# Performance work log

Hardware: AMD Instinct MI355X
Metric: run time of the kernel (lower is better)

Reference implementation:

```python
import jax, jax.numpy as jnp
import numpy as np

N = 500_000   # nodes
E = 16_000_000  # edges
G = 5_000     # graphs
H = 64        # hidden_channels
BN_EPS = 1e-5


def setup_inputs() -> dict:
    key = jax.random.key(0)
    ks = jax.random.split(key, 8)
    f32 = jnp.float32
    return {
        "x": jax.random.normal(ks[0], (N, 4), f32),
        "eps": jnp.zeros((), f32),
        "w1": jax.random.normal(ks[1], (4, 2 * H), f32) * 0.5,
        "b1": jnp.zeros((2 * H,), f32),
        "g1": jnp.ones((2 * H,), f32),
        "be1": jnp.zeros((2 * H,), f32),
        "m1": jnp.zeros((2 * H,), f32),
        "v1": jnp.ones((2 * H,), f32),
        "w2": jax.random.normal(ks[2], (2 * H, H), f32) * 0.1,
        "b2": jnp.zeros((H,), f32),
        "g2": jnp.ones((H,), f32),
        "be2": jnp.zeros((H,), f32),
        "m2": jnp.zeros((H,), f32),
        "v2": jnp.ones((H,), f32),
        "w3": jax.random.normal(ks[3], (H, 2), f32) * 0.1,
        "b3": jnp.zeros((2,), f32),
        "edge_index": jax.random.randint(ks[4], (2, E), 0, N, dtype=jnp.int64) if jax.config.jax_enable_x64 else jax.random.randint(ks[4], (2, E), 0, N, dtype=jnp.int32),
        "batch": jnp.sort(jax.random.randint(ks[5], (N,), 0, G, dtype=jnp.int32)),
    }


def _bn_eval(h, g, be, m, v):
    # BatchNorm1d in eval mode: affine transform with running stats
    return (h - m) * (g * jax.lax.rsqrt(v + BN_EPS)) + be


def reference(x, eps, w1, b1, g1, be1, m1, v1, w2, b2, g2, be2, m2, v2,
              w3, b3, edge_index, batch):
    src, dst = edge_index[0], edge_index[1]
    # GINConv: h_i = nn((1+eps)*x_i + sum_{j->i} x_j)   (adj_t @ x)
    agg = jax.ops.segment_sum(x[src], dst, num_segments=N)  # [N,4]
    h = (1.0 + eps) * x + agg
    # MLP: Linear-BN-ReLU-Linear-BN-ReLU
    h = jax.nn.relu(_bn_eval(h @ w1 + b1, g1, be1, m1, v1))   # [N,128]
    h = jax.nn.relu(_bn_eval(h @ w2 + b2, g2, be2, m2, v2))   # [N,64]
    # dropout is identity at inference
    # global_mean_pool over graphs
    sums = jax.ops.segment_sum(h, batch, num_segments=G)      # [G,64]
    cnt = jax.ops.segment_sum(jnp.ones((N, 1), h.dtype), batch, num_segments=G)
    pooled = sums / jnp.maximum(cnt, 1.0)
    logits = pooled @ w3 + b3                                 # [G,2]
    return jax.nn.log_softmax(logits, axis=-1)
```

## Files before the change

### kernel.cpp

```cpp
#include <hip/hip_runtime.h>
#include <hip/hip_fp16.h>

#define N_NODES  500000
#define N_EDGES  16000000
#define N_GRAPHS 5000

#define NBIN  512
#define BSZN  1024
#define CH    16384
#define NCH   977

#define FXS   262144.0f
#define FXI   3.814697265625e-06f

#define WS_AGG     0
#define WS_SUMS    2000000
#define WS_CNT     2320000
#define WS_W1F     2325008
#define WS_B1F     2325520
#define WS_W2F     2325648
#define WS_B2F     2333840
#define WS_HIST    2333904
#define WS_XH      WS_HIST
#define WS_BTOT    3334352
#define WS_BSTART  3334864
#define WS_CSR     3335377
#define WS_TOTAL_ELEMS 19335377

typedef __attribute__((ext_vector_type(8))) short short8;
typedef __attribute__((ext_vector_type(4))) float f32x4;

static __device__ __forceinline__ unsigned short bf16r(float f) {
    unsigned int u = __float_as_uint(f);
    u = u + 0x7FFFu + ((u >> 16) & 1u);
    return (unsigned short)(u >> 16);
}

__global__ void k_prep(const float* __restrict__ w1, const float* __restrict__ b1,
                       const float* __restrict__ g1, const float* __restrict__ be1,
                       const float* __restrict__ m1, const float* __restrict__ v1,
                       const float* __restrict__ w2, const float* __restrict__ b2,
                       const float* __restrict__ g2, const float* __restrict__ be2,
                       const float* __restrict__ m2, const float* __restrict__ v2,
                       float* __restrict__ ws) {
    int t = threadIdx.x;
    if (t < 128) {
        float s = g1[t] * rsqrtf(v1[t] + 1e-5f);
        ws[WS_B1F + t] = (b1[t] - m1[t]) * s + be1[t];
        for (int c = 0; c < 4; ++c)
            ws[WS_W1F + t * 4 + c] = w1[c * 128 + t] * s;
    }
    if (t < 64) {
        float s = g2[t] * rsqrtf(v2[t] + 1e-5f);
        ws[WS_B2F + t] = (b2[t] - m2[t]) * s + be2[t];
        unsigned short* w2t = (unsigned short*)(ws + WS_W2F);
        for (int j = 0; j < 128; ++j)
            w2t[t * 128 + j] = bf16r(w2[j * 64 + t] * s);
    }
}

__global__ __launch_bounds__(256) void k_xhalf(const float4* __restrict__ x4,
                                               uint2* __restrict__ xh) {
    int i = blockIdx.x * 256 + threadIdx.x;
    if (i >= N_NODES) return;
    float4 v = x4[i];
    __half2 a = __floats2half2_rn(v.x, v.y);
    __half2 b = __floats2half2_rn(v.z, v.w);
    uint2 p;
    p.x = *(unsigned int*)&a;
    p.y = *(unsigned int*)&b;
    xh[i] = p;
}

__global__ __launch_bounds__(256) void k_e1_hist(const int* __restrict__ ei,
                                                 int* __restrict__ hist) {
    __shared__ int h[NBIN];
    int t = threadIdx.x, blk = blockIdx.x;
    for (int i = t; i < NBIN; i += 256) h[i] = 0;
    __syncthreads();
    int base = blk * CH;
    int nE = min(CH, N_EDGES - base);
    const int4* d4 = (const int4*)(ei + N_EDGES + base);
    for (int i = t; i < (nE >> 2); i += 256) {
        int4 d = d4[i];
        atomicAdd(&h[d.x >> 10], 1);
        atomicAdd(&h[d.y >> 10], 1);
        atomicAdd(&h[d.z >> 10], 1);
        atomicAdd(&h[d.w >> 10], 1);
    }
    __syncthreads();
    for (int i = t; i < NBIN; i += 256) hist[blk * NBIN + i] = h[i];
}

__global__ __launch_bounds__(256) void k_e2a_scan(int* __restrict__ hist,
                                                  int* __restrict__ binTotal) {
    __shared__ int buf[NCH];
    int t = threadIdx.x, bin = blockIdx.x;
    for (int i = t; i < NCH; i += 256) buf[i] = hist[i * NBIN + bin];
    __syncthreads();
    if (t == 0) {
        int run = 0;
        for (int i = 0; i < NCH; ++i) { int v = buf[i]; buf[i] = run; run += v; }
        binTotal[bin] = run;
    }
    __syncthreads();
    for (int i = t; i < NCH; i += 256) hist[i * NBIN + bin] = buf[i];
}

__global__ __launch_bounds__(256) void k_e2b_scan(const int* __restrict__ binTotal,
                                                  int* __restrict__ binStart) {
    __shared__ int buf[NBIN];
    int t = threadIdx.x;
    for (int i = t; i < NBIN; i += 256) buf[i] = binTotal[i];
    __syncthreads();
    if (t == 0) {
        int run = 0;
        for (int i = 0; i < NBIN; ++i) { int v = buf[i]; buf[i] = run; run += v; }
        binStart[NBIN] = run;
    }
    __syncthreads();
    for (int i = t; i < NBIN; i += 256) binStart[i] = buf[i];
}

#define E3T 512
__global__ __launch_bounds__(E3T) void k_e3_sort(const int* __restrict__ ei,
                                                 const int* __restrict__ hist,
                                                 const int* __restrict__ binStart,
                                                 unsigned int* __restrict__ csr) {
    __shared__ unsigned int ebuf[CH];
    __shared__ int lhist[NBIN];
    __shared__ int lbase[NBIN];
    __shared__ int gbase[NBIN];
    __shared__ int cursor[NBIN];
    __shared__ int wtot[8], woff[8];
    int t = threadIdx.x, c = blockIdx.x;

    lhist[t] = 0;
    __syncthreads();

    int base = c * CH;
    int nE = min(CH, N_EDGES - base);
    for (int i = t; i < nE; i += E3T) {
        int d = ei[N_EDGES + base + i];
        atomicAdd(&lhist[d >> 10], 1);
    }
    __syncthreads();
    int v = lhist[t];
    int inc = v;
    #pragma unroll
    for (int dlt = 1; dlt < 64; dlt <<= 1) {
        int n = __shfl_up(inc, dlt, 64);
        if ((t & 63) >= dlt) inc += n;
    }
    if ((t & 63) == 63) wtot[t >> 6] = inc;
    __syncthreads();
    if (t == 0) { int r = 0; for (int w = 0; w < 8; ++w) { woff[w] = r; r += wtot[w]; } }
    __syncthreads();
    int excl = inc - v + woff[t >> 6];
    lbase[t]  = excl;
    cursor[t] = excl;
    gbase[t]  = binStart[t] + hist[c * NBIN + t];
    __syncthreads();
    for (int i = t; i < nE; i += E3T) {
        int e = base + i;
        int s = ei[e];
        int d = ei[N_EDGES + e];
        int bin = d >> 10;
        int pos = atomicAdd(&cursor[bin], 1);
        ebuf[pos] = ((unsigned int)s << 10) | (unsigned int)(d & 1023u);
    }
    __syncthreads();
    int grp = t >> 5, lane = t & 31;
    for (int b = grp; b < NBIN; b += 16) {
        int n  = lhist[b];
        int lb = lbase[b];
        int gb = gbase[b];
        for (int j = lane; j < n; j += 32)
            csr[gb + j] = ebuf[lb + j];
    }
}

__global__ __launch_bounds__(1024) void k_e4_agg(const unsigned int* __restrict__ csr,
                                                 const int* __restrict__ binStart,
                                                 const uint2* __restrict__ xh,
                                                 float* __restrict__ agg) {
    __shared__ int aggs_i[BSZN * 4];
    int t = threadIdx.x, bin = blockIdx.x;
    for (int i = t; i < BSZN * 4; i += 1024) aggs_i[i] = 0;
    __syncthreads();
    int start = binStart[bin];
    int end   = binStart[bin + 1];
    #pragma unroll 4
    for (int e = start + t; e < end; e += 1024) {
        unsigned int v = __builtin_nontemporal_load(&csr[e]);
        int src = (int)(v >> 10);
        int loc = (int)(v & 1023u);
        uint2 p = xh[src];
        __half2 ab = *(__half2*)&p.x;
        __half2 cd = *(__half2*)&p.y;
        float2 f0 = __half22float2(ab);
        float2 f1 = __half22float2(cd);
        atomicAdd(&aggs_i[0 * BSZN + loc], __float2int_rn(f0.x * FXS));
        atomicAdd(&aggs_i[1 * BSZN + loc], __float2int_rn(f0.y * FXS));
        atomicAdd(&aggs_i[2 * BSZN + loc], __float2int_rn(f1.x * FXS));
        atomicAdd(&aggs_i[3 * BSZN + loc], __float2int_rn(f1.y * FXS));
    }
    __syncthreads();
    int nodeBase = bin * BSZN;
    if (nodeBase >= N_NODES) return;
    int nv = min(BSZN, N_NODES - nodeBase) * 4;
    for (int i = t; i < nv; i += 1024) {
        int loc = i >> 2, c = i & 3;
        agg[nodeBase * 4 + i] = (float)aggs_i[c * BSZN + loc] * FXI;
    }
}

__global__ __launch_bounds__(256) void k_edge(const int* __restrict__ ei,
                                              const float4* __restrict__ x4,
                                              float* __restrict__ agg) {
    int e = blockIdx.x * 256 + threadIdx.x;
    if (e >= N_EDGES) return;
    int s = ei[e];
    int d = ei[N_EDGES + e];
    float4 v = x4[s];
    atomicAdd(&agg[d * 4 + 0], v.x);
    atomicAdd(&agg[d * 4 + 1], v.y);
    atomicAdd(&agg[d * 4 + 2], v.z);
    atomicAdd(&agg[d * 4 + 3], v.w);
}

__global__ __launch_bounds__(512) void k_node(const float4* __restrict__ x4,
                                              const float4* __restrict__ agg4,
                                              const int* __restrict__ batch,
                                              const float* __restrict__ epsp,
                                              const float* __restrict__ ws,
                                              float* __restrict__ sums,
                                              float* __restrict__ cnt) {
    __shared__ float w1s4[4 * 516];
    __shared__ float b1s[128];
    __shared__ float b2s[64];
    __shared__ float h2t[8][16][68];
    __shared__ int   bshW[128];

    int tid  = threadIdx.x;
    int wave = tid >> 6;
    int l    = tid & 63;
    int cl   = l & 15;
    int q8   = l >> 4;

    for (int i = tid; i < 2048; i += 512)
        w1s4[(i >> 9) * 516 + (i & 511)] = ws[WS_W1F + (i & 511)];
    if (tid < 128) b1s[tid] = ws[WS_B1F + tid];
    if (tid < 64)  b2s[tid] = ws[WS_B2F + tid];

    const unsigned short* w2t = (const unsigned short*)(ws + WS_W2F);
    short8 bfr[4][4];
    #pragma unroll
    for (int nt = 0; nt < 4; ++nt)
        #pragma unroll
        for (int ks = 0; ks < 4; ++ks)
            bfr[nt][ks] = *(const short8*)(w2t + (nt * 16 + cl) * 128 + ks * 32 + q8 * 8);

    __syncthreads();

    int tilebase = blockIdx.x * 128 + wave * 16;
    int node = tilebase + cl;
    bool valid = node < N_NODES;
    float4 xi = valid ? x4[node]   : make_float4(0.f, 0.f, 0.f, 0.f);
    float4 ai = valid ? agg4[node] : make_float4(0.f, 0.f, 0.f, 0.f);
    int bn = valid ? batch[node] : -1;
    if (l < 16) bshW[wave * 16 + l] = bn;
    float ep = 1.0f + epsp[0];
    float hx = ep * xi.x + ai.x;
    float hy = ep * xi.y + ai.y;
    float hz = ep * xi.z + ai.z;
    float hw = ep * xi.w + ai.w;

    f32x4 acc[4];
    #pragma unroll
    for (int nt = 0; nt < 4; ++nt) acc[nt] = (f32x4){0.f, 0.f, 0.f, 0.f};

    #pragma unroll
    for (int ks = 0; ks < 4; ++ks) {
        short8 afrag;
        #pragma unroll
        for (int e = 0; e < 8; ++e) {
            int j = ks * 32 + q8 * 8 + e;
            const float4 wr = *(const float4*)&w1s4[q8 * 516 + j * 4];
            float h1 = fmaf(hx, wr.x, fmaf(hy, wr.y, fmaf(hz, wr.z, fmaf(hw, wr.w, b1s[j]))));
            h1 = fmaxf(h1, 0.0f);
            afrag[e] = (short)bf16r(h1);
        }
        #pragma unroll
        for (int nt = 0; nt < 4; ++nt)
            acc[nt] = __builtin_amdgcn_mfma_f32_16x16x32_bf16(afrag, bfr[nt][ks], acc[nt], 0, 0, 0);
    }

    float h2v[4][4];
    #pragma unroll
    for (int nt = 0; nt < 4; ++nt) {
        float b2v = b2s[nt * 16 + cl];
        #pragma unroll
        for (int r = 0; r < 4; ++r)
            h2v[nt][r] = fmaxf(acc[nt][r] + b2v, 0.0f);
    }

    int firstb = __shfl(bn, 0);
    bool uni = __all(bn == firstb) && (firstb >= 0);
    if (uni) {
        float s[4];
        #pragma unroll
        for (int nt = 0; nt < 4; ++nt) {
            float v = h2v[nt][0] + h2v[nt][1] + h2v[nt][2] + h2v[nt][3];
            v += __shfl_xor(v, 16);
            v += __shfl_xor(v, 32);
            s[nt] = v;
        }
        if (l < 16) {
            #pragma unroll
            for (int nt = 0; nt < 4; ++nt)
                atomicAdd(&sums[firstb * 64 + nt * 16 + l], s[nt]);
        }
        if (l == 0) atomicAdd(&cnt[firstb], 16.0f);
    } else {
        #pragma unroll
        for (int nt = 0; nt < 4; ++nt)
            #pragma unroll
            for (int r = 0; r < 4; ++r)
                h2t[wave][q8 * 4 + r][nt * 16 + cl] = h2v[nt][r];
        int kout = l;
        float a = 0.f, c = 0.f;
        int cur = -1;
        for (int n = 0; n < 16; ++n) {
            int bn2 = bshW[wave * 16 + n];
            if (bn2 != cur) {
                if (cur >= 0) {
                    atomicAdd(&sums[cur * 64 + kout], a);
                    if (l == 0) atomicAdd(&cnt[cur], c);
                }
                a = 0.f; c = 0.f; cur = bn2;
            }
            if (bn2 >= 0) { a += h2t[wave][n][kout]; c += 1.f; }
        }
        if (cur >= 0) {
            atomicAdd(&sums[cur * 64 + kout], a);
            if (l == 0) atomicAdd(&cnt[cur], c);
        }
    }
}

__global__ __launch_bounds__(256) void k_head(const float* __restrict__ sums,
                                              const float* __restrict__ cnt,
                                              const float* __restrict__ w3,
                                              const float* __restrict__ b3,
                                              float* __restrict__ out) {
    int g = blockIdx.x * 256 + threadIdx.x;
    if (g >= N_GRAPHS) return;
    float ic = 1.0f / fmaxf(cnt[g], 1.0f);
    float l0 = b3[0], l1 = b3[1];
    #pragma unroll 8
    for (int k = 0; k < 64; ++k) {
        float p = sums[g * 64 + k] * ic;
        l0 = fmaf(p, w3[k * 2 + 0], l0);
        l1 = fmaf(p, w3[k * 2 + 1], l1);
    }
    float m = fmaxf(l0, l1);
    float lse = m + logf(expf(l0 - m) + expf(l1 - m));
    out[g * 2 + 0] = l0 - lse;
    out[g * 2 + 1] = l1 - lse;
}

extern "C" void kernel_launch(void* const* d_in, const int* in_sizes, int n_in,
                              void* d_out, int out_size, void* d_ws, size_t ws_size,
                              hipStream_t stream) {
    const float* x   = (const float*)d_in[0];
    const float* eps = (const float*)d_in[1];
    const float* w1  = (const float*)d_in[2];
    const float* b1  = (const float*)d_in[3];
    const float* g1  = (const float*)d_in[4];
    const float* be1 = (const float*)d_in[5];
    const float* m1  = (const float*)d_in[6];
    const float* v1  = (const float*)d_in[7];
    const float* w2  = (const float*)d_in[8];
    const float* b2  = (const float*)d_in[9];
    const float* g2  = (const float*)d_in[10];
    const float* be2 = (const float*)d_in[11];
    const float* m2  = (const float*)d_in[12];
    const float* v2  = (const float*)d_in[13];
    const float* w3  = (const float*)d_in[14];
    const float* b3  = (const float*)d_in[15];
    const int*   ei  = (const int*)d_in[16];
    const int*   batch = (const int*)d_in[17];

    float* ws = (float*)d_ws;
    int*   wsi = (int*)d_ws;

    k_prep<<<1, 128, 0, stream>>>(w1, b1, g1, be1, m1, v1, w2, b2, g2, be2, m2, v2, ws);

    if (ws_size >= (size_t)WS_TOTAL_ELEMS * 4) {
        hipMemsetAsync(ws + WS_SUMS, 0, (size_t)(320000 + 5000) * sizeof(float), stream);

        k_e1_hist<<<NCH, 256, 0, stream>>>(ei, wsi + WS_HIST);
        k_e2a_scan<<<NBIN, 256, 0, stream>>>(wsi + WS_HIST, wsi + WS_BTOT);
        k_e2b_scan<<<1, 256, 0, stream>>>(wsi + WS_BTOT, wsi + WS_BSTART);
        k_e3_sort<<<NCH, E3T, 0, stream>>>(ei, wsi + WS_HIST, wsi + WS_BSTART,
                                           (unsigned int*)(wsi + WS_CSR));
        k_xhalf<<<(N_NODES + 255) / 256, 256, 0, stream>>>((const float4*)x,
                                                           (uint2*)(wsi + WS_XH));
        k_e4_agg<<<NBIN, 1024, 0, stream>>>((const unsigned int*)(wsi + WS_CSR),
                                            wsi + WS_BSTART,
                                            (const uint2*)(wsi + WS_XH), ws + WS_AGG);
    } else {
        hipMemsetAsync(ws, 0, (size_t)(2000000 + 320000 + 5000) * sizeof(float), stream);
        k_edge<<<(N_EDGES + 255) / 256, 256, 0, stream>>>(ei, (const float4*)x, ws + WS_AGG);
    }

    k_node<<<(N_NODES + 127) / 128, 512, 0, stream>>>(
        (const float4*)x, (const float4*)(ws + WS_AGG), batch, eps, ws,
        ws + WS_SUMS, ws + WS_CNT);

    k_head<<<(N_GRAPHS + 255) / 256, 256, 0, stream>>>(
        ws + WS_SUMS, ws + WS_CNT, w3, b3, (float*)d_out);
}
```

Baseline: 309.0 us.

## Replace per-chunk histogram scan with atomic bin totals and global cursors

The per-chunk bin histogram matrix and its column-wise serial scan kernel are removed. The histogram kernel now atomically accumulates global bin totals, a single parallel-scan kernel computes bin starts and cursors, and each sort block claims its slice of every bin with an atomicAdd on the global cursor. This drops one kernel launch and the strided scan over 977x512 counts, but makes edge order within a bin nondeterministic, which is harmless because aggregation uses integer atomics. The aggregation loop unroll also rises from 4 to 8.

Result: slower. 318.6 us (+3.1%).

```diff
diff --git a/kernel.cpp b/kernel.cpp
--- a/kernel.cpp
+++ b/kernel.cpp
@@ -20,12 +20,12 @@
 #define WS_B1F     2325520
 #define WS_W2F     2325648
 #define WS_B2F     2333840
-#define WS_HIST    2333904
-#define WS_XH      WS_HIST
-#define WS_BTOT    3334352
-#define WS_BSTART  3334864
-#define WS_CSR     3335377
-#define WS_TOTAL_ELEMS 19335377
+#define WS_XH      2333904
+#define WS_BTOT    3333904
+#define WS_BSTART  3334416
+#define WS_GCUR    3334929
+#define WS_CSR     3335441
+#define WS_TOTAL_ELEMS 19335441
 
 typedef __attribute__((ext_vector_type(8))) short short8;
 typedef __attribute__((ext_vector_type(4))) float f32x4;
@@ -44,6 +44,8 @@
                        const float* __restrict__ m2, const float* __restrict__ v2,
                        float* __restrict__ ws) {
     int t = threadIdx.x;
+    int* wsi = (int*)ws;
+    for (int i = t; i < NBIN; i += 128) wsi[WS_BTOT + i] = 0;
     if (t < 128) {
         float s = g1[t] * rsqrtf(v1[t] + 1e-5f);
         ws[WS_B1F + t] = (b1[t] - m1[t]) * s + be1[t];
@@ -72,8 +74,8 @@
     xh[i] = p;
 }
 
-__global__ __launch_bounds__(256) void k_e1_hist(const int* __restrict__ ei,
-                                                 int* __restrict__ hist) {
+__global__ __launch_bounds__(256) void k_hist(const int* __restrict__ ei,
+                                              int* __restrict__ binTotal) {
     __shared__ int h[NBIN];
     int t = threadIdx.x, blk = blockIdx.x;
     for (int i = t; i < NBIN; i += 256) h[i] = 0;
@@ -89,43 +91,35 @@
         atomicAdd(&h[d.w >> 10], 1);
     }
     __syncthreads();
-    for (int i = t; i < NBIN; i += 256) hist[blk * NBIN + i] = h[i];
-}
-
-__global__ __launch_bounds__(256) void k_e2a_scan(int* __restrict__ hist,
-                                                  int* __restrict__ binTotal) {
-    __shared__ int buf[NCH];
-    int t = threadIdx.x, bin = blockIdx.x;
-    for (int i = t; i < NCH; i += 256) buf[i] = hist[i * NBIN + bin];
-    __syncthreads();
-    if (t == 0) {
-        int run = 0;
-        for (int i = 0; i < NCH; ++i) { int v = buf[i]; buf[i] = run; run += v; }
-        binTotal[bin] = run;
-    }
-    __syncthreads();
-    for (int i = t; i < NCH; i += 256) hist[i * NBIN + bin] = buf[i];
-}
-
-__global__ __launch_bounds__(256) void k_e2b_scan(const int* __restrict__ binTotal,
-                                                  int* __restrict__ binStart) {
-    __shared__ int buf[NBIN];
+    for (int i = t; i < NBIN; i += 256)
+        if (h[i]) atomicAdd(&binTotal[i], h[i]);
+}
+
+__global__ __launch_bounds__(512) void k_scan(const int* __restrict__ binTotal,
+                                              int* __restrict__ binStart,
+                                              int* __restrict__ gcur) {
+    __shared__ int wtot[8], woff[8];
     int t = threadIdx.x;
-    for (int i = t; i < NBIN; i += 256) buf[i] = binTotal[i];
-    __syncthreads();
-    if (t == 0) {
-        int run = 0;
-        for (int i = 0; i < NBIN; ++i) { int v = buf[i]; buf[i] = run; run += v; }
-        binStart[NBIN] = run;
-    }
-    __syncthreads();
-    for (int i = t; i < NBIN; i += 256) binStart[i] = buf[i];
+    int v = binTotal[t];
+    int inc = v;
+    #pragma unroll
+    for (int dlt = 1; dlt < 64; dlt <<= 1) {
+        int n = __shfl_up(inc, dlt, 64);
+        if ((t & 63) >= dlt) inc += n;
+    }
+    if ((t & 63) == 63) wtot[t >> 6] = inc;
+    __syncthreads();
+    if (t == 0) { int r = 0; for (int w = 0; w < 8; ++w) { woff[w] = r; r += wtot[w]; } }
+    __syncthreads();
+    int excl = inc - v + woff[t >> 6];
+    binStart[t] = excl;
+    gcur[t] = excl;
+    if (t == NBIN - 1) binStart[NBIN] = excl + v;
 }
 
 #define E3T 512
 __global__ __launch_bounds__(E3T) void k_e3_sort(const int* __restrict__ ei,
-                                                 const int* __restrict__ hist,
-                                                 const int* __restrict__ binStart,
+                                                 int* __restrict__ gcur,
                                                  unsigned int* __restrict__ csr) {
     __shared__ unsigned int ebuf[CH];
     __shared__ int lhist[NBIN];
@@ -159,7 +153,7 @@
     int excl = inc - v + woff[t >> 6];
     lbase[t]  = excl;
     cursor[t] = excl;
-    gbase[t]  = binStart[t] + hist[c * NBIN + t];
+    gbase[t] = v ? atomicAdd(&gcur[t], v) : 0;
     __syncthreads();
     for (int i = t; i < nE; i += E3T) {
         int e = base + i;
@@ -190,7 +184,7 @@
     __syncthreads();
     int start = binStart[bin];
     int end   = binStart[bin + 1];
-    #pragma unroll 4
+    #pragma unroll 8
     for (int e = start + t; e < end; e += 1024) {
         unsigned int v = __builtin_nontemporal_load(&csr[e]);
         int src = (int)(v >> 10);
@@ -400,13 +394,12 @@
     if (ws_size >= (size_t)WS_TOTAL_ELEMS * 4) {
         hipMemsetAsync(ws + WS_SUMS, 0, (size_t)(320000 + 5000) * sizeof(float), stream);
 
-        k_e1_hist<<<NCH, 256, 0, stream>>>(ei, wsi + WS_HIST);
-        k_e2a_scan<<<NBIN, 256, 0, stream>>>(wsi + WS_HIST, wsi + WS_BTOT);
-        k_e2b_scan<<<1, 256, 0, stream>>>(wsi + WS_BTOT, wsi + WS_BSTART);
-        k_e3_sort<<<NCH, E3T, 0, stream>>>(ei, wsi + WS_HIST, wsi + WS_BSTART,
-                                           (unsigned int*)(wsi + WS_CSR));
         k_xhalf<<<(N_NODES + 255) / 256, 256, 0, stream>>>((const float4*)x,
                                                            (uint2*)(wsi + WS_XH));
+        k_hist<<<NCH, 256, 0, stream>>>(ei, wsi + WS_BTOT);
+        k_scan<<<1, 512, 0, stream>>>(wsi + WS_BTOT, wsi + WS_BSTART, wsi + WS_GCUR);
+        k_e3_sort<<<NCH, E3T, 0, stream>>>(ei, wsi + WS_GCUR,
+                                           (unsigned int*)(wsi + WS_CSR));
         k_e4_agg<<<NBIN, 1024, 0, stream>>>((const unsigned int*)(wsi + WS_CSR),
                                             wsi + WS_BSTART,
                                             (const uint2*)(wsi + WS_XH), ws + WS_AGG);
```

## Halve sort chunks, parallelize scans, vectorize sort loads, split aggregation blocks

Applied to the files above, without the earlier changes.

Edge chunk size is halved so the histogram and sort stages launch twice as many blocks. The two serial single-thread prefix scans become wave-shuffle scans. The sort kernel now reads src/dst as int4, and the aggregation kernel splits each destination bin across two blocks that merge fixed-point partial sums with global integer atomics. The cost is a larger memset to zero the integer aggregation buffer, plus extra global atomics.

Result: faster. 289.4 us (-6.4%).

```diff
diff --git a/kernel.cpp b/kernel.cpp
--- a/kernel.cpp
+++ b/kernel.cpp
@@ -7,8 +7,8 @@
 
 #define NBIN  512
 #define BSZN  1024
-#define CH    16384
-#define NCH   977
+#define CH    8192
+#define NCH   1954
 
 #define FXS   262144.0f
 #define FXI   3.814697265625e-06f
@@ -94,32 +94,51 @@
 
 __global__ __launch_bounds__(256) void k_e2a_scan(int* __restrict__ hist,
                                                   int* __restrict__ binTotal) {
-    __shared__ int buf[NCH];
+    __shared__ int buf[2048];
+    __shared__ int wsum[4], woff2[4];
     int t = threadIdx.x, bin = blockIdx.x;
-    for (int i = t; i < NCH; i += 256) buf[i] = hist[i * NBIN + bin];
-    __syncthreads();
-    if (t == 0) {
-        int run = 0;
-        for (int i = 0; i < NCH; ++i) { int v = buf[i]; buf[i] = run; run += v; }
-        binTotal[bin] = run;
-    }
-    __syncthreads();
+    for (int i = t; i < 2048; i += 256)
+        buf[i] = (i < NCH) ? hist[i * NBIN + bin] : 0;
+    __syncthreads();
+    int s = 0;
+    #pragma unroll
+    for (int k = 0; k < 8; ++k) s += buf[t * 8 + k];
+    int inc = s;
+    #pragma unroll
+    for (int dlt = 1; dlt < 64; dlt <<= 1) {
+        int n = __shfl_up(inc, dlt, 64);
+        if ((t & 63) >= dlt) inc += n;
+    }
+    if ((t & 63) == 63) wsum[t >> 6] = inc;
+    __syncthreads();
+    if (t == 0) { int r = 0; for (int w = 0; w < 4; ++w) { woff2[w] = r; r += wsum[w]; } }
+    __syncthreads();
+    int run = inc - s + woff2[t >> 6];
+    #pragma unroll
+    for (int k = 0; k < 8; ++k) { int v = buf[t * 8 + k]; buf[t * 8 + k] = run; run += v; }
+    __syncthreads();
+    if (t == 0) binTotal[bin] = woff2[3] + wsum[3];
     for (int i = t; i < NCH; i += 256) hist[i * NBIN + bin] = buf[i];
 }
 
-__global__ __launch_bounds__(256) void k_e2b_scan(const int* __restrict__ binTotal,
+__global__ __launch_bounds__(512) void k_e2b_scan(const int* __restrict__ binTotal,
                                                   int* __restrict__ binStart) {
-    __shared__ int buf[NBIN];
+    __shared__ int wtot[8], woff[8];
     int t = threadIdx.x;
-    for (int i = t; i < NBIN; i += 256) buf[i] = binTotal[i];
-    __syncthreads();
-    if (t == 0) {
-        int run = 0;
-        for (int i = 0; i < NBIN; ++i) { int v = buf[i]; buf[i] = run; run += v; }
-        binStart[NBIN] = run;
-    }
-    __syncthreads();
-    for (int i = t; i < NBIN; i += 256) binStart[i] = buf[i];
+    int v = binTotal[t];
+    int inc = v;
+    #pragma unroll
+    for (int dlt = 1; dlt < 64; dlt <<= 1) {
+        int n = __shfl_up(inc, dlt, 64);
+        if ((t & 63) >= dlt) inc += n;
+    }
+    if ((t & 63) == 63) wtot[t >> 6] = inc;
+    __syncthreads();
+    if (t == 0) { int r = 0; for (int w = 0; w < 8; ++w) { woff[w] = r; r += wtot[w]; } }
+    __syncthreads();
+    int excl = inc - v + woff[t >> 6];
+    binStart[t] = excl;
+    if (t == NBIN - 1) binStart[NBIN] = excl + v;
 }
 
 #define E3T 512
@@ -129,7 +148,6 @@
                                                  unsigned int* __restrict__ csr) {
     __shared__ unsigned int ebuf[CH];
     __shared__ int lhist[NBIN];
-    __shared__ int lbase[NBIN];
     __shared__ int gbase[NBIN];
     __shared__ int cursor[NBIN];
     __shared__ int wtot[8], woff[8];
@@ -140,9 +158,15 @@
 
     int base = c * CH;
     int nE = min(CH, N_EDGES - base);
-    for (int i = t; i < nE; i += E3T) {
-        int d = ei[N_EDGES + base + i];
-        atomicAdd(&lhist[d >> 10], 1);
+    {
+        const int4* d4 = (const int4*)(ei + N_EDGES + base);
+        for (int i = t; i < (nE >> 2); i += E3T) {
+            int4 d = d4[i];
+            atomicAdd(&lhist[d.x >> 10], 1);
+            atomicAdd(&lhist[d.y >> 10], 1);
+            atomicAdd(&lhist[d.z >> 10], 1);
+            atomicAdd(&lhist[d.w >> 10], 1);
+        }
     }
     __syncthreads();
     int v = lhist[t];
@@ -157,25 +181,32 @@
     if (t == 0) { int r = 0; for (int w = 0; w < 8; ++w) { woff[w] = r; r += wtot[w]; } }
     __syncthreads();
     int excl = inc - v + woff[t >> 6];
-    lbase[t]  = excl;
     cursor[t] = excl;
     gbase[t]  = binStart[t] + hist[c * NBIN + t];
     __syncthreads();
-    for (int i = t; i < nE; i += E3T) {
-        int e = base + i;
-        int s = ei[e];
-        int d = ei[N_EDGES + e];
-        int bin = d >> 10;
-        int pos = atomicAdd(&cursor[bin], 1);
-        ebuf[pos] = ((unsigned int)s << 10) | (unsigned int)(d & 1023u);
-    }
-    __syncthreads();
-    int grp = t >> 5, lane = t & 31;
-    for (int b = grp; b < NBIN; b += 16) {
+    {
+        const int4* s4 = (const int4*)(ei + base);
+        const int4* d4 = (const int4*)(ei + N_EDGES + base);
+        for (int i = t; i < (nE >> 2); i += E3T) {
+            int4 s = s4[i];
+            int4 d = d4[i];
+            int p0 = atomicAdd(&cursor[d.x >> 10], 1);
+            ebuf[p0] = ((unsigned int)s.x << 10) | (unsigned int)(d.x & 1023);
+            int p1 = atomicAdd(&cursor[d.y >> 10], 1);
+            ebuf[p1] = ((unsigned int)s.y << 10) | (unsigned int)(d.y & 1023);
+            int p2 = atomicAdd(&cursor[d.z >> 10], 1);
+            ebuf[p2] = ((unsigned int)s.z << 10) | (unsigned int)(d.z & 1023);
+            int p3 = atomicAdd(&cursor[d.w >> 10], 1);
+            ebuf[p3] = ((unsigned int)s.w << 10) | (unsigned int)(d.w & 1023);
+        }
+    }
+    __syncthreads();
+    int grp = t >> 4, lane = t & 15;
+    for (int b = grp; b < NBIN; b += (E3T / 16)) {
         int n  = lhist[b];
-        int lb = lbase[b];
+        int lb = cursor[b] - n;
         int gb = gbase[b];
-        for (int j = lane; j < n; j += 32)
+        for (int j = lane; j < n; j += 16)
             csr[gb + j] = ebuf[lb + j];
     }
 }
@@ -183,14 +214,19 @@
 __global__ __launch_bounds__(1024) void k_e4_agg(const unsigned int* __restrict__ csr,
                                                  const int* __restrict__ binStart,
                                                  const uint2* __restrict__ xh,
-                                                 float* __restrict__ agg) {
+                                                 int* __restrict__ aggi) {
     __shared__ int aggs_i[BSZN * 4];
-    int t = threadIdx.x, bin = blockIdx.x;
+    int t = threadIdx.x;
+    int bin  = blockIdx.x >> 1;
+    int half = blockIdx.x & 1;
     for (int i = t; i < BSZN * 4; i += 1024) aggs_i[i] = 0;
     __syncthreads();
-    int start = binStart[bin];
-    int end   = binStart[bin + 1];
-    #pragma unroll 4
+    int s0 = binStart[bin];
+    int e0 = binStart[bin + 1];
+    int mid = s0 + ((e0 - s0) >> 1);
+    int start = half ? mid : s0;
+    int end   = half ? e0  : mid;
+    #pragma unroll 8
     for (int e = start + t; e < end; e += 1024) {
         unsigned int v = __builtin_nontemporal_load(&csr[e]);
         int src = (int)(v >> 10);
@@ -210,27 +246,29 @@
     if (nodeBase >= N_NODES) return;
     int nv = min(BSZN, N_NODES - nodeBase) * 4;
     for (int i = t; i < nv; i += 1024) {
-        int loc = i >> 2, c = i & 3;
-        agg[nodeBase * 4 + i] = (float)aggs_i[c * BSZN + loc] * FXI;
+        int pv = aggs_i[(i & 3) * BSZN + (i >> 2)];
+        if (pv) atomicAdd(&aggi[nodeBase * 4 + i], pv);
     }
 }
 
 __global__ __launch_bounds__(256) void k_edge(const int* __restrict__ ei,
                                               const float4* __restrict__ x4,
-                                              float* __restrict__ agg) {
+                                              float* __restrict__ aggf) {
     int e = blockIdx.x * 256 + threadIdx.x;
     if (e >= N_EDGES) return;
     int s = ei[e];
     int d = ei[N_EDGES + e];
     float4 v = x4[s];
-    atomicAdd(&agg[d * 4 + 0], v.x);
-    atomicAdd(&agg[d * 4 + 1], v.y);
-    atomicAdd(&agg[d * 4 + 2], v.z);
-    atomicAdd(&agg[d * 4 + 3], v.w);
+    atomicAdd(&aggf[d * 4 + 0], v.x);
+    atomicAdd(&aggf[d * 4 + 1], v.y);
+    atomicAdd(&aggf[d * 4 + 2], v.z);
+    atomicAdd(&aggf[d * 4 + 3], v.w);
 }
 
 __global__ __launch_bounds__(512) void k_node(const float4* __restrict__ x4,
-                                              const float4* __restrict__ agg4,
+                                              const int* __restrict__ aggi,
+                                              const float* __restrict__ aggf,
+                                              int useFix,
                                               const int* __restrict__ batch,
                                               const float* __restrict__ epsp,
                                               const float* __restrict__ ws,
@@ -266,8 +304,16 @@
     int tilebase = blockIdx.x * 128 + wave * 16;
     int node = tilebase + cl;
     bool valid = node < N_NODES;
-    float4 xi = valid ? x4[node]   : make_float4(0.f, 0.f, 0.f, 0.f);
-    float4 ai = valid ? agg4[node] : make_float4(0.f, 0.f, 0.f, 0.f);
+    float4 xi = valid ? x4[node] : make_float4(0.f, 0.f, 0.f, 0.f);
+    float4 ai;
+    if (valid) {
+        if (useFix) {
+            int4 av = ((const int4*)aggi)[node];
+            ai = make_float4(av.x * FXI, av.y * FXI, av.z * FXI, av.w * FXI);
+        } else {
+            ai = ((const float4*)aggf)[node];
+        }
+    } else ai = make_float4(0.f, 0.f, 0.f, 0.f);
     int bn = valid ? batch[node] : -1;
     if (l < 16) bshW[wave * 16 + l] = bn;
     float ep = 1.0f + epsp[0];
@@ -398,26 +444,31 @@
     k_prep<<<1, 128, 0, stream>>>(w1, b1, g1, be1, m1, v1, w2, b2, g2, be2, m2, v2, ws);
 
     if (ws_size >= (size_t)WS_TOTAL_ELEMS * 4) {
-        hipMemsetAsync(ws + WS_SUMS, 0, (size_t)(320000 + 5000) * sizeof(float), stream);
+        hipMemsetAsync(ws, 0, (size_t)2325000 * sizeof(float), stream);
 
         k_e1_hist<<<NCH, 256, 0, stream>>>(ei, wsi + WS_HIST);
         k_e2a_scan<<<NBIN, 256, 0, stream>>>(wsi + WS_HIST, wsi + WS_BTOT);
-        k_e2b_scan<<<1, 256, 0, stream>>>(wsi + WS_BTOT, wsi + WS_BSTART);
+        k_e2b_scan<<<1, NBIN, 0, stream>>>(wsi + WS_BTOT, wsi + WS_BSTART);
         k_e3_sort<<<NCH, E3T, 0, stream>>>(ei, wsi + WS_HIST, wsi + WS_BSTART,
                                            (unsigned int*)(wsi + WS_CSR));
         k_xhalf<<<(N_NODES + 255) / 256, 256, 0, stream>>>((const float4*)x,
                                                            (uint2*)(wsi + WS_XH));
-        k_e4_agg<<<NBIN, 1024, 0, stream>>>((const unsigned int*)(wsi + WS_CSR),
-                                            wsi + WS_BSTART,
-                                            (const uint2*)(wsi + WS_XH), ws + WS_AGG);
+        k_e4_agg<<<NBIN * 2, 1024, 0, stream>>>((const unsigned int*)(wsi + WS_CSR),
+                                                wsi + WS_BSTART,
+                                                (const uint2*)(wsi + WS_XH),
+                                                wsi + WS_AGG);
+        k_node<<<(N_NODES + 127) / 128, 512, 0, stream>>>(
+            (const float4*)x, wsi + WS_AGG, (const float*)nullptr, 1, batch, eps, ws,
+            ws + WS_SUMS, ws + WS_CNT);
     } else {
-        hipMemsetAsync(ws, 0, (size_t)(2000000 + 320000 + 5000) * sizeof(float), stream);
-        k_edge<<<(N_EDGES + 255) / 256, 256, 0, stream>>>(ei, (const float4*)x, ws + WS_AGG);
-    }
-
-    k_node<<<(N_NODES + 127) / 128, 512, 0, stream>>>(
-        (const float4*)x, (const float4*)(ws + WS_AGG), batch, eps, ws,
-        ws + WS_SUMS, ws + WS_CNT);
+        hipMemsetAsync(ws + WS_SUMS, 0, (size_t)325000 * sizeof(float), stream);
+        hipMemsetAsync(ws + WS_CSR, 0, (size_t)2000000 * sizeof(float), stream);
+        k_edge<<<(N_EDGES + 255) / 256, 256, 0, stream>>>(ei, (const float4*)x,
+                                                          ws + WS_CSR);
+        k_node<<<(N_NODES + 127) / 128, 512, 0, stream>>>(
+            (const float4*)x, (const int*)nullptr, ws + WS_CSR, 0, batch, eps, ws,
+            ws + WS_SUMS, ws + WS_CNT);
+    }
 
     k_head<<<(N_GRAPHS + 255) / 256, 256, 0, stream>>>(
         ws + WS_SUMS, ws + WS_CNT, w3, b3, (float*)d_out);
```
